# Performance work log

Measured on AMD Instinct MI355X. Metric: run time of the kernel, lower is better.

Reference implementation:

```python
import jax, jax.numpy as jnp
import numpy as np
from jax import lax

BETA = 0.25            # commitment_beta (multiplies code_book_loss per source)
CODEBOOK_WEIGHT = 1.0  # multiplies commitment_loss per source
GN_GROUPS = 8
GN_EPS = 1e-5


def conv2d(x, w, b):
    # 3x3 same-padding conv, NCHW / OIHW
    y = lax.conv_general_dilated(x, w, (1, 1), [(1, 1), (1, 1)],
                                 dimension_numbers=('NCHW', 'OIHW', 'NCHW'))
    return y + b[None, :, None, None]


def group_norm(x, scale, bias):
    B, C, H, W = x.shape
    xg = x.reshape(B, GN_GROUPS, C // GN_GROUPS, H, W)
    mean = xg.mean(axis=(2, 3, 4), keepdims=True)
    var = xg.var(axis=(2, 3, 4), keepdims=True)
    xg = (xg - mean) * lax.rsqrt(var + GN_EPS)
    x = xg.reshape(B, C, H, W)
    return x * scale[None, :, None, None] + bias[None, :, None, None]


def setup_inputs() -> dict:
    key = jax.random.key(0)
    ks = jax.random.split(key, 4)
    x = jax.random.normal(ks[0], (8, 3, 64, 64), jnp.float32)
    conv_in_w = jax.random.normal(ks[1], (64, 3, 3, 3), jnp.float32) * 0.1
    conv_in_b = jnp.zeros((64,), jnp.float32)
    codebook = jax.random.normal(ks[2], (4096, 64), jnp.float32) * 0.5
    gn_scale = jnp.ones((64,), jnp.float32)
    gn_bias = jnp.zeros((64,), jnp.float32)
    dec_w = jax.random.normal(ks[3], (3, 64, 3, 3), jnp.float32) * 0.1
    dec_b = jnp.zeros((3,), jnp.float32)
    return {"x": x, "conv_in_w": conv_in_w, "conv_in_b": conv_in_b,
            "codebook": codebook, "gn_scale": gn_scale, "gn_bias": gn_bias,
            "dec_w": dec_w, "dec_b": dec_b}


def reference(x, conv_in_w, conv_in_b, codebook, gn_scale, gn_bias, dec_w, dec_b):
    # Encoder: channels=[64], mid_layers=[64] => just conv_in
    feat = conv2d(x, conv_in_w, conv_in_b)          # [B,64,H,W]
    B, C, H, W = feat.shape

    # quantize(): cdist -> argmin -> gather -> losses -> straight-through
    quant_in = feat.transpose(0, 2, 3, 1).reshape(B, H * W, C)  # [B,n,C]
    # squared euclidean distances (argmin identical to torch.cdist p=2 argmin)
    d = ((quant_in ** 2).sum(-1, keepdims=True)
         - 2.0 * jnp.einsum('bnc,kc->bnk', quant_in, codebook)
         + (codebook ** 2).sum(-1)[None, None, :])              # [B,n,K]
    min_idx = jnp.argmin(d, axis=-1)                            # [B,n]
    quant_out = codebook[min_idx.reshape(-1)]                   # [B*n,C]
    qi_flat = quant_in.reshape(-1, C)                            # [B*n,C]

    commitment_loss = CODEBOOK_WEIGHT * jnp.mean(
        (lax.stop_gradient(quant_out) - qi_flat) ** 2)
    code_book_loss = BETA * jnp.mean(
        (lax.stop_gradient(qi_flat) - quant_out) ** 2)

    st = qi_flat + lax.stop_gradient(quant_out - qi_flat)        # straight-through
    quant_nchw = st.reshape(B, H, W, C).transpose(0, 3, 1, 2)

    # Decoder: channels=[64] => norm_out + silu + decoder_out
    out = group_norm(quant_nchw, gn_scale, gn_bias)
    out = jax.nn.silu(out)
    reconstruction = conv2d(out, dec_w, dec_b)                   # [B,3,H,W]
    return reconstruction, quant_nchw, commitment_loss, code_book_loss
```

## Files before the change

### kernel.cpp

```cpp
#include <hip/hip_runtime.h>
#include <hip/hip_bf16.h>

typedef __attribute__((ext_vector_type(8))) short short8;
typedef __attribute__((ext_vector_type(4))) float f32x4;

#define KK 4096
#define NELEM 2097152
#define TAU 0.004f
#define RESCUE_CAP 8192

__device__ __forceinline__ unsigned short f2bf(float f) {
    unsigned u = __float_as_uint(f);
    u = (u + 0x7FFFu + ((u >> 16) & 1u)) >> 16;
    return (unsigned short)u;
}
__device__ __forceinline__ float bf2f(unsigned short h) {
    return __uint_as_float(((unsigned)h) << 16);
}

__global__ void k_prep(const float* __restrict__ cb, float* __restrict__ cn,
                       unsigned short* __restrict__ cbh, unsigned short* __restrict__ cbl) {
    int t = blockIdx.x * 256 + threadIdx.x;
    int row = t >> 2, part = t & 3;
    const float4* p = (const float4*)(cb + (size_t)row * 64 + part * 16);
    float s = 0.f;
    short8 hv[2], lv[2];
#pragma unroll
    for (int i = 0; i < 4; i++) {
        float4 v = p[i];
        float arr[4] = {v.x, v.y, v.z, v.w};
#pragma unroll
        for (int j = 0; j < 4; j++) {
            float f = arr[j];
            s += f * f;
            int e = i * 4 + j;
            unsigned short h = f2bf(f);
            hv[e >> 3][e & 7] = (short)h;
            lv[e >> 3][e & 7] = (short)f2bf(f - bf2f(h));
        }
    }
    short8* oh = (short8*)(cbh + (size_t)row * 64 + part * 16);
    short8* ol = (short8*)(cbl + (size_t)row * 64 + part * 16);
    oh[0] = hv[0]; oh[1] = hv[1];
    ol[0] = lv[0]; ol[1] = lv[1];
    s += __shfl_xor(s, 1, 64);
    s += __shfl_xor(s, 2, 64);
    if (part == 0) cn[row] = s;
}

#define MFMA __builtin_amdgcn_mfma_f32_16x16x32_bf16

__global__ __launch_bounds__(256, 2) void k_argmin(
    const float* __restrict__ x, const float* __restrict__ ciw, const float* __restrict__ cib,
    const unsigned short* __restrict__ cbh, const unsigned short* __restrict__ cbl,
    const float* __restrict__ cn, const float* __restrict__ cb,
    float* __restrict__ quant, float* __restrict__ ssd,
    float* __restrict__ gsum, float* __restrict__ gsq,
    unsigned int* __restrict__ rcnt, int* __restrict__ rlist) {

    __shared__ float    slab[3][3][66];
    __shared__ unsigned qtile[64][65];
    __shared__ float    mb1[4][64];
    __shared__ float    mb2[4][64];
    __shared__ int      mi1[4][64];
    __shared__ int      fi[64];
    __shared__ float    gred[4][16];

    const int tid = threadIdx.x;
    const int L   = tid & 63;
    const int wv  = tid >> 6;
    const int blk = blockIdx.x;
    const int b   = blk >> 6, h = blk & 63;

    for (int idx = tid; idx < 594; idx += 256) {
        int ci = idx / 198, rem = idx - ci * 198;
        int kh = rem / 66,  colp = rem - kh * 66;
        int hh = h + kh - 1, ww = colp - 1;
        float v = 0.f;
        if (hh >= 0 && hh < 64 && ww >= 0 && ww < 64)
            v = x[((b * 3 + ci) << 12) + (hh << 6) + ww];
        slab[ci][kh][colp] = v;
    }
    __syncthreads();

    {
        const int w_  = L;
        const int cgs = __builtin_amdgcn_readfirstlane(wv);
        float xv[27];
#pragma unroll
        for (int ci = 0; ci < 3; ci++)
#pragma unroll
            for (int kh = 0; kh < 3; kh++)
#pragma unroll
                for (int kw = 0; kw < 3; kw++)
                    xv[ci * 9 + kh * 3 + kw] = slab[ci][kh][w_ + kw];
#pragma unroll
        for (int j = 0; j < 16; j++) {
            int co = cgs * 16 + j;
            float acc = cib[co];
#pragma unroll
            for (int t2 = 0; t2 < 27; t2++)
                acc = fmaf(xv[t2], ciw[co * 27 + t2], acc);
            unsigned short hbits = f2bf(acc);
            unsigned short lbits = f2bf(acc - bf2f(hbits));
            qtile[w_][co] = (unsigned)hbits | ((unsigned)lbits << 16);
        }
    }
    __syncthreads();

    const int col = L & 15, g = L >> 4;
    short8 qh[4][2], ql[4][2];
#pragma unroll
    for (int mt = 0; mt < 4; mt++) {
        int qrow = mt * 16 + col;
#pragma unroll
        for (int kh = 0; kh < 2; kh++) {
            int d0 = (kh * 4 + g) * 8;
#pragma unroll
            for (int e = 0; e < 8; e++) {
                unsigned u = qtile[qrow][d0 + e];
                qh[mt][kh][e] = (short)(u & 0xFFFFu);
                ql[mt][kh][e] = (short)(u >> 16);
            }
        }
    }

    float vb1[4][4], vb2[4][4];
    int   vi1[4][4];
#pragma unroll
    for (int mt = 0; mt < 4; mt++)
#pragma unroll
        for (int e = 0; e < 4; e++) { vb1[mt][e] = 3.4e38f; vb2[mt][e] = 3.4e38f; vi1[mt][e] = 0; }

    const int cbase0 = wv << 10;
    const unsigned short* ph = cbh + (size_t)(cbase0 + col) * 64;
    const unsigned short* pl = cbl + (size_t)(cbase0 + col) * 64;

    short8 c0h0, c0h1, c0l0, c0l1, c1h0, c1h1, c1l0, c1l1;

    auto LD = [&](int gi, short8& h0, short8& h1, short8& l0, short8& l1) {
        const short8* p0 = (const short8*)(ph + ((size_t)gi << 10));
        const short8* p1 = (const short8*)(pl + ((size_t)gi << 10));
        h0 = p0[g]; h1 = p0[4 + g]; l0 = p1[g]; l1 = p1[4 + g];
    };
    auto PROC = [&](int gi, short8& h0, short8& h1, short8& l0, short8& l1) {
        int   kvb = cbase0 + gi * 16 + col;
        float cnk = cn[kvb];
#pragma unroll
        for (int mt = 0; mt < 4; mt++) {
            f32x4 acc = {0.f, 0.f, 0.f, 0.f};
            acc = MFMA(qh[mt][0], h0, acc, 0, 0, 0);
            acc = MFMA(qh[mt][1], h1, acc, 0, 0, 0);
            acc = MFMA(qh[mt][0], l0, acc, 0, 0, 0);
            acc = MFMA(qh[mt][1], l1, acc, 0, 0, 0);
            acc = MFMA(ql[mt][0], h0, acc, 0, 0, 0);
            acc = MFMA(ql[mt][1], h1, acc, 0, 0, 0);
#pragma unroll
            for (int e = 0; e < 4; e++) {
                float s = fmaf(acc[e], -2.f, cnk);
                vb2[mt][e] = __builtin_amdgcn_fmed3f(s, vb1[mt][e], vb2[mt][e]);
                bool take = s < vb1[mt][e];
                vi1[mt][e] = take ? kvb : vi1[mt][e];
                vb1[mt][e] = take ? s : vb1[mt][e];
            }
        }
    };

    LD(0, c0h0, c0h1, c0l0, c0l1);
#pragma unroll 1
    for (int gi = 0; gi < 64; gi += 2) {
        LD(gi + 1, c1h0, c1h1, c1l0, c1l1);
        PROC(gi, c0h0, c0h1, c0l0, c0l1);
        int gn = gi + 2 <= 63 ? gi + 2 : 63;
        LD(gn, c0h0, c0h1, c0l0, c0l1);
        PROC(gi + 1, c1h0, c1h1, c1l0, c1l1);
    }

#pragma unroll
    for (int mt = 0; mt < 4; mt++)
#pragma unroll
    for (int e = 0; e < 4; e++) {
        float b1 = vb1[mt][e], b2 = vb2[mt][e];
        int i1 = vi1[mt][e];
#pragma unroll
        for (int m = 1; m < 16; m <<= 1) {
            float ob1 = __shfl_xor(b1, m, 64);
            float ob2 = __shfl_xor(b2, m, 64);
            int   oi1 = __shfl_xor(i1, m, 64);
            float hi = fmaxf(b1, ob1);
            b2 = fminf(fminf(b2, ob2), hi);
            bool take = (ob1 < b1) || ((ob1 == b1) && (oi1 < i1));
            if (take) { b1 = ob1; i1 = oi1; }
        }
        if (col == 0) {
            int qloc = mt * 16 + g * 4 + e;
            mb1[wv][qloc] = b1; mb2[wv][qloc] = b2; mi1[wv][qloc] = i1;
        }
    }
    __syncthreads();

    if (tid < 64) {
        float b1 = mb1[0][tid], b2 = mb2[0][tid];
        int i1 = mi1[0][tid];
#pragma unroll
        for (int w2 = 1; w2 < 4; w2++) {
            float ob1 = mb1[w2][tid], ob2 = mb2[w2][tid];
            int   oi1 = mi1[w2][tid];
            float hi = fmaxf(b1, ob1);
            b2 = fminf(fminf(b2, ob2), hi);
            bool take = (ob1 < b1) || ((ob1 == b1) && (oi1 < i1));
            if (take) { b1 = ob1; i1 = oi1; }
        }
        fi[tid] = i1;
        if (b2 - b1 < TAU) {
            unsigned pos = atomicAdd(rcnt, 1u);
            if (pos < RESCUE_CAP) {
                rlist[2 * pos] = blk * 64 + tid;
                rlist[2 * pos + 1] = i1;
            }
        }
    }
    __syncthreads();

    {
        int qloc = tid >> 2, part = tid & 3;
        int idx = fi[qloc];
        int q = blk * 64 + qloc;
        int hw = q & 4095;
        const float* crow = cb + (size_t)idx * 64 + part * 16;
        float* qout = quant + ((size_t)b << 18) + ((size_t)(part * 16) << 12) + hw;
        float ps = 0.f, sA = 0.f, sA2 = 0.f, sB = 0.f, sB2 = 0.f;
#pragma unroll
        for (int cc = 0; cc < 16; cc++) {
            unsigned u = qtile[qloc][part * 16 + cc];
            float fv = bf2f((unsigned short)(u & 0xFFFFu)) + bf2f((unsigned short)(u >> 16));
            float cv = crow[cc];
            float d = cv - fv;
            ps += d * d;
            if (cc < 8) { sA += cv; sA2 += cv * cv; } else { sB += cv; sB2 += cv * cv; }
            qout[(size_t)cc << 12] = cv;
        }
#pragma unroll
        for (int off = 32; off; off >>= 1) ps += __shfl_down(ps, off, 64);
        if (L == 0) atomicAdd(ssd, ps);
#pragma unroll
        for (int m = 4; m <= 32; m <<= 1) {
            sA  += __shfl_xor(sA, m, 64);  sA2 += __shfl_xor(sA2, m, 64);
            sB  += __shfl_xor(sB, m, 64);  sB2 += __shfl_xor(sB2, m, 64);
        }
        if (L < 4) {
            gred[wv][L * 4 + 0] = sA;  gred[wv][L * 4 + 1] = sA2;
            gred[wv][L * 4 + 2] = sB;  gred[wv][L * 4 + 3] = sB2;
        }
    }
    __syncthreads();
    if (tid < 16) {
        float v = gred[0][tid] + gred[1][tid] + gred[2][tid] + gred[3][tid];
        int part = tid >> 2, stat = tid & 3;
        int grp = b * 8 + part * 2 + (stat >> 1);
        atomicAdd((stat & 1) ? &gsq[grp] : &gsum[grp], v);
    }
}

__global__ void k_rescue(const int* __restrict__ rlist, const unsigned int* __restrict__ rcnt,
                         const float* __restrict__ x, const float* __restrict__ ciw,
                         const float* __restrict__ cib,
                         const float* __restrict__ cb, const float* __restrict__ cn,
                         float* __restrict__ quant, float* __restrict__ ssd,
                         float* __restrict__ gsum, float* __restrict__ gsq) {
    __shared__ float fqs[64];
    __shared__ float rb[4];
    __shared__ int   ri[4];
    __shared__ int   s_new;
    int tid = threadIdx.x;
    unsigned cnt = *rcnt;
    int n = (int)(cnt > RESCUE_CAP ? RESCUE_CAP : cnt);
    for (int r = blockIdx.x; r < n; r += gridDim.x) {
        int q = rlist[2 * r], old_i = rlist[2 * r + 1];
        int b = q >> 12, h = (q >> 6) & 63, w_ = q & 63;
        if (tid < 64) {
            float acc = cib[tid];
#pragma unroll
            for (int ci = 0; ci < 3; ci++)
#pragma unroll
            for (int kh = 0; kh < 3; kh++) {
                int hh = h + kh - 1;
                if (hh < 0 || hh >= 64) continue;
#pragma unroll
                for (int kw = 0; kw < 3; kw++) {
                    int ww = w_ + kw - 1;
                    if (ww < 0 || ww >= 64) continue;
                    acc = fmaf(x[((b * 3 + ci) << 12) + (hh << 6) + ww],
                               ciw[tid * 27 + ci * 9 + kh * 3 + kw], acc);
                }
            }
            fqs[tid] = acc;
        }
        __syncthreads();
        float best = 3.4e38f; int bi = 0;
        for (int kk = 0; kk < 16; kk++) {
            int k = kk * 256 + tid;
            const float4* cp = (const float4*)(cb + (size_t)k * 64);
            float d0 = 0.f, d1 = 0.f, d2 = 0.f, d3 = 0.f;
#pragma unroll
            for (int i = 0; i < 16; i += 4) {
                float4 c0 = cp[i], c1 = cp[i+1], c2 = cp[i+2], c3 = cp[i+3];
                d0 += fqs[4*i+ 0]*c0.x + fqs[4*i+ 1]*c0.y + fqs[4*i+ 2]*c0.z + fqs[4*i+ 3]*c0.w;
                d1 += fqs[4*i+ 4]*c1.x + fqs[4*i+ 5]*c1.y + fqs[4*i+ 6]*c1.z + fqs[4*i+ 7]*c1.w;
                d2 += fqs[4*i+ 8]*c2.x + fqs[4*i+ 9]*c2.y + fqs[4*i+10]*c2.z + fqs[4*i+11]*c2.w;
                d3 += fqs[4*i+12]*c3.x + fqs[4*i+13]*c3.y + fqs[4*i+14]*c3.z + fqs[4*i+15]*c3.w;
            }
            float s = cn[k] - 2.f * ((d0 + d1) + (d2 + d3));
            if (s < best) { best = s; bi = k; }
        }
#pragma unroll
        for (int off = 32; off; off >>= 1) {
            float ob = __shfl_down(best, off, 64);
            int   oi = __shfl_down(bi, off, 64);
            if (ob < best || (ob == best && oi < bi)) { best = ob; bi = oi; }
        }
        if ((tid & 63) == 0) { rb[tid >> 6] = best; ri[tid >> 6] = bi; }
        __syncthreads();
        if (tid == 0) {
            float bb = rb[0]; int ii = ri[0];
#pragma unroll
            for (int w2 = 1; w2 < 4; w2++)
                if (rb[w2] < bb || (rb[w2] == bb && ri[w2] < ii)) { bb = rb[w2]; ii = ri[w2]; }
            s_new = ii;
        }
        __syncthreads();
        int ni = s_new;
        if (ni != old_i && tid < 64) {
            float fv = fqs[tid];
            float co_ = cb[(size_t)old_i * 64 + tid];
            float cw  = cb[(size_t)ni * 64 + tid];
            quant[((size_t)b << 18) + ((size_t)tid << 12) + (q & 4095)] = cw;
            float dssd = (cw - fv) * (cw - fv) - (co_ - fv) * (co_ - fv);
            float ds  = cw - co_;
            float ds2 = cw * cw - co_ * co_;
#pragma unroll
            for (int off = 32; off; off >>= 1) dssd += __shfl_down(dssd, off, 64);
#pragma unroll
            for (int m = 1; m < 8; m <<= 1) {
                ds  += __shfl_xor(ds, m, 64);
                ds2 += __shfl_xor(ds2, m, 64);
            }
            if (tid == 0) atomicAdd(ssd, dssd);
            if ((tid & 7) == 0) {
                atomicAdd(&gsum[b * 8 + (tid >> 3)], ds);
                atomicAdd(&gsq [b * 8 + (tid >> 3)], ds2);
            }
        }
        __syncthreads();
    }
}

__global__ void k_norm_silu(const float* __restrict__ quant,
                            const float* __restrict__ gsum, const float* __restrict__ gsq,
                            const float* __restrict__ scale, const float* __restrict__ bias,
                            float* __restrict__ normed) {
    int t = blockIdx.x * 256 + threadIdx.x;
    int c = (t >> 10) & 63;
    int b = t >> 16;
    int grp = b * 8 + (c >> 3);
    float m = gsum[grp] * (1.f / 32768.f);
    float var = gsq[grp] * (1.f / 32768.f) - m * m;
    float r = rsqrtf(var + 1e-5f);
    float sc = scale[c] * r;
    float bi = bias[c] - m * sc;
    float4 v = ((const float4*)quant)[t];
    float4 o;
    float y;
    y = v.x * sc + bi; o.x = y / (1.f + expf(-y));
    y = v.y * sc + bi; o.y = y / (1.f + expf(-y));
    y = v.z * sc + bi; o.z = y / (1.f + expf(-y));
    y = v.w * sc + bi; o.w = y / (1.f + expf(-y));
    ((float4*)normed)[t] = o;
}

__global__ void k_conv_out(const float* __restrict__ normed, const float* __restrict__ w,
                           const float* __restrict__ bias, float* __restrict__ out) {
    int blk = blockIdx.x;
    int h = blk & 63;
    int t2 = blk >> 6;
    int co = t2 % 3, b = t2 / 3;
    int tid = threadIdx.x;
    int ciq = tid & 3, w_ = tid >> 2;
    float acc = 0.f;
    const float* wt = w + (size_t)(co * 64 + ciq * 16) * 9;
    const float* np = normed + ((size_t)(b * 64 + ciq * 16) << 12);
#pragma unroll 4
    for (int cj = 0; cj < 16; cj++) {
#pragma unroll
        for (int kh = 0; kh < 3; kh++) {
            int hh = h + kh - 1;
            if (hh < 0 || hh >= 64) continue;
            const float* row = np + ((size_t)cj << 12) + (hh << 6);
            float wk0 = wt[cj * 9 + kh * 3 + 0];
            float wk1 = wt[cj * 9 + kh * 3 + 1];
            float wk2 = wt[cj * 9 + kh * 3 + 2];
            if (w_ > 0)  acc = fmaf(row[w_ - 1], wk0, acc);
            acc = fmaf(row[w_], wk1, acc);
            if (w_ < 63) acc = fmaf(row[w_ + 1], wk2, acc);
        }
    }
    acc += __shfl_xor(acc, 1, 64);
    acc += __shfl_xor(acc, 2, 64);
    if (ciq == 0)
        out[((size_t)(b * 3 + co) << 12) + (h << 6) + w_] = acc + bias[co];
}

__global__ void k_loss(const float* __restrict__ ssd, float* __restrict__ losses) {
    float mean = ssd[0] / 2097152.f;
    losses[0] = mean;
    losses[1] = 0.25f * mean;
}

extern "C" void kernel_launch(void* const* d_in, const int* in_sizes, int n_in,
                              void* d_out, int out_size, void* d_ws, size_t ws_size,
                              hipStream_t stream) {
    const float* x   = (const float*)d_in[0];
    const float* ciw = (const float*)d_in[1];
    const float* cib = (const float*)d_in[2];
    const float* cb  = (const float*)d_in[3];
    const float* gsc = (const float*)d_in[4];
    const float* gbi = (const float*)d_in[5];
    const float* dw  = (const float*)d_in[6];
    const float* db  = (const float*)d_in[7];

    float* out = (float*)d_out;
    char* wsb  = (char*)d_ws;

    float*          ssd   = (float*)wsb;
    unsigned int*   rcnt  = (unsigned int*)(wsb + 4);
    float*          gsum  = (float*)(wsb + 64);
    float*          gsq   = (float*)(wsb + 320);
    float*          cn    = (float*)(wsb + 1024);
    int*            rlist = (int*)(wsb + 65536);
    unsigned short* cbh   = (unsigned short*)(wsb + 131072);
    unsigned short* cbl   = (unsigned short*)(wsb + 655360);
    float*          normed = (float*)(wsb + 1179648);

    float* recon  = out;
    float* quant  = out + 98304;
    float* losses = out + 98304 + NELEM;

    hipMemsetAsync(wsb, 0, 1024, stream);
    k_prep     <<<64,   256, 0, stream>>>(cb, cn, cbh, cbl);
    k_argmin   <<<512,  256, 0, stream>>>(x, ciw, cib, cbh, cbl, cn, cb,
                                          quant, ssd, gsum, gsq, rcnt, rlist);
    k_rescue   <<<128,  256, 0, stream>>>(rlist, rcnt, x, ciw, cib, cb, cn,
                                          quant, ssd, gsum, gsq);
    k_norm_silu<<<2048, 256, 0, stream>>>(quant, gsum, gsq, gsc, gbi, normed);
    k_conv_out <<<1536, 256, 0, stream>>>(normed, dw, db, recon);
    k_loss     <<<1,    1,   0, stream>>>(ssd, losses);
}
```

Baseline: 302.9 us.

## Widen argmin to 8 waves, fuse norm-silu into output conv, tighten rescue threshold

The argmin kernel now uses 512 threads per block, so each of 8 waves scans 512 codebook entries instead of 1024, and the conv-in and epilogue work is split across 8 waves. GroupNorm+SiLU is fused into the decoder conv, which stages normalized rows in shared memory, removing the intermediate normed buffer round-trip and one launch. The rescue margin TAU drops from 0.004 to 0.001 so fewer near-tie queries get rechecked, and rescue gets more blocks. The smaller TAU risks missing argmin mismatches from the bf16 split-precision distances, and the higher occupancy target may limit registers.

```diff
diff --git a/kernel.cpp b/kernel.cpp
--- a/kernel.cpp
+++ b/kernel.cpp
@@ -6,7 +6,7 @@
 
 #define KK 4096
 #define NELEM 2097152
-#define TAU 0.004f
+#define TAU 0.001f
 #define RESCUE_CAP 8192
 
 __device__ __forceinline__ unsigned short f2bf(float f) {
@@ -50,7 +50,7 @@
 
 #define MFMA __builtin_amdgcn_mfma_f32_16x16x32_bf16
 
-__global__ __launch_bounds__(256, 2) void k_argmin(
+__global__ __launch_bounds__(512, 4) void k_argmin(
     const float* __restrict__ x, const float* __restrict__ ciw, const float* __restrict__ cib,
     const unsigned short* __restrict__ cbh, const unsigned short* __restrict__ cbl,
     const float* __restrict__ cn, const float* __restrict__ cb,
@@ -60,11 +60,11 @@
 
     __shared__ float    slab[3][3][66];
     __shared__ unsigned qtile[64][65];
-    __shared__ float    mb1[4][64];
-    __shared__ float    mb2[4][64];
-    __shared__ int      mi1[4][64];
+    __shared__ float    mb1[8][64];
+    __shared__ float    mb2[8][64];
+    __shared__ int      mi1[8][64];
     __shared__ int      fi[64];
-    __shared__ float    gred[4][16];
+    __shared__ float    gred[8][16];
 
     const int tid = threadIdx.x;
     const int L   = tid & 63;
@@ -72,7 +72,7 @@
     const int blk = blockIdx.x;
     const int b   = blk >> 6, h = blk & 63;
 
-    for (int idx = tid; idx < 594; idx += 256) {
+    for (int idx = tid; idx < 594; idx += 512) {
         int ci = idx / 198, rem = idx - ci * 198;
         int kh = rem / 66,  colp = rem - kh * 66;
         int hh = h + kh - 1, ww = colp - 1;
@@ -95,8 +95,8 @@
                 for (int kw = 0; kw < 3; kw++)
                     xv[ci * 9 + kh * 3 + kw] = slab[ci][kh][w_ + kw];
 #pragma unroll
-        for (int j = 0; j < 16; j++) {
-            int co = cgs * 16 + j;
+        for (int j = 0; j < 8; j++) {
+            int co = cgs * 8 + j;
             float acc = cib[co];
 #pragma unroll
             for (int t2 = 0; t2 < 27; t2++)
@@ -132,7 +132,7 @@
 #pragma unroll
         for (int e = 0; e < 4; e++) { vb1[mt][e] = 3.4e38f; vb2[mt][e] = 3.4e38f; vi1[mt][e] = 0; }
 
-    const int cbase0 = wv << 10;
+    const int cbase0 = wv << 9;
     const unsigned short* ph = cbh + (size_t)(cbase0 + col) * 64;
     const unsigned short* pl = cbl + (size_t)(cbase0 + col) * 64;
 
@@ -168,10 +168,10 @@
 
     LD(0, c0h0, c0h1, c0l0, c0l1);
 #pragma unroll 1
-    for (int gi = 0; gi < 64; gi += 2) {
+    for (int gi = 0; gi < 32; gi += 2) {
         LD(gi + 1, c1h0, c1h1, c1l0, c1l1);
         PROC(gi, c0h0, c0h1, c0l0, c0l1);
-        int gn = gi + 2 <= 63 ? gi + 2 : 63;
+        int gn = gi + 2 <= 31 ? gi + 2 : 31;
         LD(gn, c0h0, c0h1, c0l0, c0l1);
         PROC(gi + 1, c1h0, c1h1, c1l0, c1l1);
     }
@@ -203,7 +203,7 @@
         float b1 = mb1[0][tid], b2 = mb2[0][tid];
         int i1 = mi1[0][tid];
 #pragma unroll
-        for (int w2 = 1; w2 < 4; w2++) {
+        for (int w2 = 1; w2 < 8; w2++) {
             float ob1 = mb1[w2][tid], ob2 = mb2[w2][tid];
             int   oi1 = mi1[w2][tid];
             float hi = fmaxf(b1, ob1);
@@ -223,42 +223,44 @@
     __syncthreads();
 
     {
-        int qloc = tid >> 2, part = tid & 3;
+        int qloc = tid >> 3, part = tid & 7;
         int idx = fi[qloc];
         int q = blk * 64 + qloc;
         int hw = q & 4095;
-        const float* crow = cb + (size_t)idx * 64 + part * 16;
-        float* qout = quant + ((size_t)b << 18) + ((size_t)(part * 16) << 12) + hw;
-        float ps = 0.f, sA = 0.f, sA2 = 0.f, sB = 0.f, sB2 = 0.f;
-#pragma unroll
-        for (int cc = 0; cc < 16; cc++) {
-            unsigned u = qtile[qloc][part * 16 + cc];
+        const float* crow = cb + (size_t)idx * 64 + part * 8;
+        float* qout = quant + ((size_t)b << 18) + ((size_t)(part * 8) << 12) + hw;
+        float ps = 0.f, sA = 0.f, sA2 = 0.f;
+#pragma unroll
+        for (int cc = 0; cc < 8; cc++) {
+            unsigned u = qtile[qloc][part * 8 + cc];
             float fv = bf2f((unsigned short)(u & 0xFFFFu)) + bf2f((unsigned short)(u >> 16));
             float cv = crow[cc];
             float d = cv - fv;
             ps += d * d;
-            if (cc < 8) { sA += cv; sA2 += cv * cv; } else { sB += cv; sB2 += cv * cv; }
+            sA += cv; sA2 += cv * cv;
             qout[(size_t)cc << 12] = cv;
         }
 #pragma unroll
         for (int off = 32; off; off >>= 1) ps += __shfl_down(ps, off, 64);
         if (L == 0) atomicAdd(ssd, ps);
 #pragma unroll
-        for (int m = 4; m <= 32; m <<= 1) {
-            sA  += __shfl_xor(sA, m, 64);  sA2 += __shfl_xor(sA2, m, 64);
-            sB  += __shfl_xor(sB, m, 64);  sB2 += __shfl_xor(sB2, m, 64);
-        }
-        if (L < 4) {
-            gred[wv][L * 4 + 0] = sA;  gred[wv][L * 4 + 1] = sA2;
-            gred[wv][L * 4 + 2] = sB;  gred[wv][L * 4 + 3] = sB2;
+        for (int m = 8; m <= 32; m <<= 1) {
+            sA  += __shfl_xor(sA, m, 64);
+            sA2 += __shfl_xor(sA2, m, 64);
+        }
+        if (L < 8) {
+            gred[wv][L * 2 + 0] = sA;
+            gred[wv][L * 2 + 1] = sA2;
         }
     }
     __syncthreads();
     if (tid < 16) {
-        float v = gred[0][tid] + gred[1][tid] + gred[2][tid] + gred[3][tid];
-        int part = tid >> 2, stat = tid & 3;
-        int grp = b * 8 + part * 2 + (stat >> 1);
-        atomicAdd((stat & 1) ? &gsq[grp] : &gsum[grp], v);
+        float v = 0.f;
+#pragma unroll
+        for (int w2 = 0; w2 < 8; w2++) v += gred[w2][tid];
+        int part = tid >> 1, stat = tid & 1;
+        int grp = b * 8 + part;
+        atomicAdd(stat ? &gsq[grp] : &gsum[grp], v);
     }
 }
 
@@ -355,59 +357,70 @@
     }
 }
 
-__global__ void k_norm_silu(const float* __restrict__ quant,
-                            const float* __restrict__ gsum, const float* __restrict__ gsq,
-                            const float* __restrict__ scale, const float* __restrict__ bias,
-                            float* __restrict__ normed) {
-    int t = blockIdx.x * 256 + threadIdx.x;
-    int c = (t >> 10) & 63;
-    int b = t >> 16;
-    int grp = b * 8 + (c >> 3);
-    float m = gsum[grp] * (1.f / 32768.f);
-    float var = gsq[grp] * (1.f / 32768.f) - m * m;
-    float r = rsqrtf(var + 1e-5f);
-    float sc = scale[c] * r;
-    float bi = bias[c] - m * sc;
-    float4 v = ((const float4*)quant)[t];
-    float4 o;
-    float y;
-    y = v.x * sc + bi; o.x = y / (1.f + expf(-y));
-    y = v.y * sc + bi; o.y = y / (1.f + expf(-y));
-    y = v.z * sc + bi; o.z = y / (1.f + expf(-y));
-    y = v.w * sc + bi; o.w = y / (1.f + expf(-y));
-    ((float4*)normed)[t] = o;
-}
-
-__global__ void k_conv_out(const float* __restrict__ normed, const float* __restrict__ w,
-                           const float* __restrict__ bias, float* __restrict__ out) {
-    int blk = blockIdx.x;
-    int h = blk & 63;
-    int t2 = blk >> 6;
-    int co = t2 % 3, b = t2 / 3;
-    int tid = threadIdx.x;
-    int ciq = tid & 3, w_ = tid >> 2;
-    float acc = 0.f;
-    const float* wt = w + (size_t)(co * 64 + ciq * 16) * 9;
-    const float* np = normed + ((size_t)(b * 64 + ciq * 16) << 12);
+__global__ __launch_bounds__(256, 2) void k_out(
+    const float* __restrict__ quant,
+    const float* __restrict__ gsum, const float* __restrict__ gsq,
+    const float* __restrict__ scale, const float* __restrict__ bias,
+    const float* __restrict__ dw, const float* __restrict__ db,
+    float* __restrict__ out) {
+
+    __shared__ float nls[64 * 3 * 66];
+    __shared__ float sc_s[64], bi_s[64];
+
+    const int tid = threadIdx.x;
+    const int blk = blockIdx.x;
+    const int b = blk >> 6, h = blk & 63;
+
+    if (tid < 64) {
+        int grp = b * 8 + (tid >> 3);
+        float m = gsum[grp] * (1.f / 32768.f);
+        float var = gsq[grp] * (1.f / 32768.f) - m * m;
+        float r = rsqrtf(var + 1e-5f);
+        float sc = scale[tid] * r;
+        sc_s[tid] = sc;
+        bi_s[tid] = bias[tid] - m * sc;
+    }
+    for (int idx = tid; idx < 384; idx += 256) {
+        int ci = idx / 6, r2 = idx % 6;
+        int kh = r2 >> 1, side = r2 & 1;
+        nls[ci * 198 + kh * 66 + (side ? 65 : 0)] = 0.f;
+    }
+    __syncthreads();
+
+#pragma unroll
+    for (int i = 0; i < 48; i++) {
+        int idx = tid + i * 256;
+        int w_ = idx & 63;
+        int t2 = idx >> 6;
+        int kh = t2 % 3, ci = t2 / 3;
+        int hh = h + kh - 1;
+        float v = 0.f;
+        if (hh >= 0 && hh < 64) {
+            float qv = quant[((size_t)(b * 64 + ci) << 12) + (hh << 6) + w_];
+            float y = qv * sc_s[ci] + bi_s[ci];
+            v = y / (1.f + expf(-y));
+        }
+        nls[ci * 198 + kh * 66 + w_ + 1] = v;
+    }
+    __syncthreads();
+
+    const int co = tid >> 6;
+    const int w_ = tid & 63;
+    if (co < 3) {
+        float acc = db[co];
 #pragma unroll 4
-    for (int cj = 0; cj < 16; cj++) {
-#pragma unroll
-        for (int kh = 0; kh < 3; kh++) {
-            int hh = h + kh - 1;
-            if (hh < 0 || hh >= 64) continue;
-            const float* row = np + ((size_t)cj << 12) + (hh << 6);
-            float wk0 = wt[cj * 9 + kh * 3 + 0];
-            float wk1 = wt[cj * 9 + kh * 3 + 1];
-            float wk2 = wt[cj * 9 + kh * 3 + 2];
-            if (w_ > 0)  acc = fmaf(row[w_ - 1], wk0, acc);
-            acc = fmaf(row[w_], wk1, acc);
-            if (w_ < 63) acc = fmaf(row[w_ + 1], wk2, acc);
-        }
-    }
-    acc += __shfl_xor(acc, 1, 64);
-    acc += __shfl_xor(acc, 2, 64);
-    if (ciq == 0)
-        out[((size_t)(b * 3 + co) << 12) + (h << 6) + w_] = acc + bias[co];
+        for (int ci = 0; ci < 64; ci++) {
+            const float* wt = dw + (size_t)(co * 64 + ci) * 9;
+#pragma unroll
+            for (int kh = 0; kh < 3; kh++) {
+                const float* base = nls + ci * 198 + kh * 66 + w_;
+                acc = fmaf(base[0], wt[kh * 3 + 0], acc);
+                acc = fmaf(base[1], wt[kh * 3 + 1], acc);
+                acc = fmaf(base[2], wt[kh * 3 + 2], acc);
+            }
+        }
+        out[((size_t)(b * 3 + co) << 12) + (h << 6) + w_] = acc;
+    }
 }
 
 __global__ void k_loss(const float* __restrict__ ssd, float* __restrict__ losses) {
@@ -439,19 +452,17 @@
     int*            rlist = (int*)(wsb + 65536);
     unsigned short* cbh   = (unsigned short*)(wsb + 131072);
     unsigned short* cbl   = (unsigned short*)(wsb + 655360);
-    float*          normed = (float*)(wsb + 1179648);
 
     float* recon  = out;
     float* quant  = out + 98304;
     float* losses = out + 98304 + NELEM;
 
     hipMemsetAsync(wsb, 0, 1024, stream);
-    k_prep     <<<64,   256, 0, stream>>>(cb, cn, cbh, cbl);
-    k_argmin   <<<512,  256, 0, stream>>>(x, ciw, cib, cbh, cbl, cn, cb,
-                                          quant, ssd, gsum, gsq, rcnt, rlist);
-    k_rescue   <<<128,  256, 0, stream>>>(rlist, rcnt, x, ciw, cib, cb, cn,
-                                          quant, ssd, gsum, gsq);
-    k_norm_silu<<<2048, 256, 0, stream>>>(quant, gsum, gsq, gsc, gbi, normed);
-    k_conv_out <<<1536, 256, 0, stream>>>(normed, dw, db, recon);
-    k_loss     <<<1,    1,   0, stream>>>(ssd, losses);
-}
+    k_prep   <<<64,   256, 0, stream>>>(cb, cn, cbh, cbl);
+    k_argmin <<<512,  512, 0, stream>>>(x, ciw, cib, cbh, cbl, cn, cb,
+                                        quant, ssd, gsum, gsq, rcnt, rlist);
+    k_rescue <<<256,  256, 0, stream>>>(rlist, rcnt, x, ciw, cib, cb, cn,
+                                        quant, ssd, gsum, gsq);
+    k_out    <<<512,  256, 0, stream>>>(quant, gsum, gsq, gsc, gbi, dw, db, recon);
+    k_loss   <<<1,    1,   0, stream>>>(ssd, losses);
+}
```

Measured after the change: 524.5 us. +73.2%, slower.
